# Kernel tuning notes

Measured on AMD Instinct MI355X. Metric: run time of the kernel, lower is better.

The kernel has to match this reference:

```python
import jax, jax.numpy as jnp
import numpy as np

D, ED, N, R, K, NL = 128, 256, 16, 8, 4, 3   # d_model, d_inner, d_state, dt_rank, d_conv, n_layers
B, L = 4, 1024
HID, OUT = 256, 2
EPS = 1e-5


def setup_inputs() -> dict:
    key = jax.random.key(0)
    ks = jax.random.split(key, 16)
    g = lambda k, shape, s=0.05: jax.random.normal(k, shape, dtype=jnp.float32) * s
    return {
        "x": jax.random.normal(ks[0], (B, L, D), dtype=jnp.float32),
        # Mamba params, stacked over (2 directions, NL layers)
        "rms_w": jnp.ones((2, NL, D), jnp.float32),
        "in_w": g(ks[1], (2, NL, 2 * ED, D)),
        "in_b": g(ks[2], (2, NL, 2 * ED)),
        "conv_w": g(ks[3], (2, NL, ED, K)),
        "conv_b": g(ks[4], (2, NL, ED)),
        "xproj_w": g(ks[5], (2, NL, R + 2 * N, ED)),
        "dt_w": g(ks[6], (2, NL, ED, R)),
        "dt_b": g(ks[7], (2, NL, ED)),
        "A_log": jnp.broadcast_to(jnp.log(jnp.arange(1.0, N + 1.0, dtype=jnp.float32)), (2, NL, ED, N)) + 0.0,
        "Dp": jnp.ones((2, NL, ED), jnp.float32),
        "out_w": g(ks[8], (2, NL, D, ED)),
        "out_b": g(ks[9], (2, NL, D)),
        # MLP head params (BatchNorm in training mode: batch stats)
        "bn1_g": jnp.ones((2 * D,), jnp.float32), "bn1_b": jnp.zeros((2 * D,), jnp.float32),
        "w1": g(ks[10], (HID, 2 * D)), "b1": g(ks[11], (HID,)),
        "bn2_g": jnp.ones((HID,), jnp.float32), "bn2_b": jnp.zeros((HID,), jnp.float32),
        "w2": g(ks[12], (HID, HID)), "b2": g(ks[13], (HID,)),
        "bn3_g": jnp.ones((HID,), jnp.float32), "bn3_b": jnp.zeros((HID,), jnp.float32),
        "w3": g(ks[14], (OUT, HID)), "b3": g(ks[15], (OUT,)),
    }


def _rms(x, w):
    return x * jax.lax.rsqrt(jnp.mean(x * x, axis=-1, keepdims=True) + EPS) * w


def _dwconv(x, w, b):
    # causal depthwise conv; x: (B,L,ED), w: (ED,K)
    y = jax.lax.conv_general_dilated(x.transpose(0, 2, 1), w[:, None, :], (1,), [(K - 1, 0)],
                                     feature_group_count=ED, dimension_numbers=("NCH", "OIH", "NCH"))
    return y.transpose(0, 2, 1) + b


def _ssm(dA, dBx, C):
    # dA,dBx: (B,L,ED,N); C: (B,L,N) -> y: (B,L,ED)
    def step(h, inp):
        a, bx, c = inp
        h = a * h + bx
        return h, jnp.einsum("ben,bn->be", h, c)
    h0 = jnp.zeros((dA.shape[0], ED, N), dA.dtype)
    _, ys = jax.lax.scan(step, h0, (dA.transpose(1, 0, 2, 3), dBx.transpose(1, 0, 2, 3), C.transpose(1, 0, 2)))
    return ys.transpose(1, 0, 2)


def _block(x, in_w, in_b, conv_w, conv_b, xproj_w, dt_w, dt_b, A_log, Dp, out_w, out_b):
    xz = x @ in_w.T + in_b
    xi, z = xz[..., :ED], xz[..., ED:]
    xi = jax.nn.silu(_dwconv(xi, conv_w, conv_b))
    dbc = xi @ xproj_w.T
    dt, Bm, Cm = dbc[..., :R], dbc[..., R:R + N], dbc[..., R + N:]
    delta = jax.nn.softplus(dt @ dt_w.T + dt_b)            # (B,L,ED)
    A = -jnp.exp(A_log)                                    # (ED,N)
    dA = jnp.exp(delta[..., None] * A)                     # (B,L,ED,N)
    dBx = (delta * xi)[..., None] * Bm[:, :, None, :]      # (B,L,ED,N)
    y = _ssm(dA, dBx, Cm) + Dp * xi
    y = y * jax.nn.silu(z)
    return y @ out_w.T + out_b


def _mamba(x, d, rms_w, in_w, in_b, conv_w, conv_b, xproj_w, dt_w, dt_b, A_log, Dp, out_w, out_b):
    for l in range(NL):
        x = x + _block(_rms(x, rms_w[d, l]), in_w[d, l], in_b[d, l], conv_w[d, l], conv_b[d, l],
                       xproj_w[d, l], dt_w[d, l], dt_b[d, l], A_log[d, l], Dp[d, l], out_w[d, l], out_b[d, l])
    return x


def _bn(x, g, b):
    m = jnp.mean(x, axis=0)
    v = jnp.mean((x - m) ** 2, axis=0)  # biased var, torch BN training mode
    return (x - m) * jax.lax.rsqrt(v + EPS) * g + b


def _forward(x, rms_w, in_w, in_b, conv_w, conv_b, xproj_w, dt_w, dt_b, A_log, Dp, out_w, out_b,
             bn1_g, bn1_b, w1, b1, bn2_g, bn2_b, w2, b2, bn3_g, bn3_b, w3, b3):
    mp = (rms_w, in_w, in_b, conv_w, conv_b, xproj_w, dt_w, dt_b, A_log, Dp, out_w, out_b)
    fwd = _mamba(x, 0, *mp)
    bwd = jnp.flip(_mamba(jnp.flip(x, axis=1), 1, *mp), axis=1)
    h = jnp.concatenate([fwd, bwd], axis=2).reshape(B * L, 2 * D)
    h = jax.nn.leaky_relu(_bn(h, bn1_g, bn1_b) @ w1.T + b1)
    h = jax.nn.leaky_relu(_bn(h, bn2_g, bn2_b) @ w2.T + b2)
    h = _bn(h, bn3_g, bn3_b) @ w3.T + b3
    return h.reshape(B, L, OUT)


def reference(x, rms_w, in_w, in_b, conv_w, conv_b, xproj_w, dt_w, dt_b, A_log, Dp, out_w, out_b,
              bn1_g, bn1_b, w1, b1, bn2_g, bn2_b, w2, b2, bn3_g, bn3_b, w3, b3):
    return _forward(x, rms_w, in_w, in_b, conv_w, conv_b, xproj_w, dt_w, dt_b, A_log, Dp, out_w, out_b,
                    bn1_g, bn1_b, w1, b1, bn2_g, bn2_b, w2, b2, bn3_g, bn3_b, w3, b3)
```

## Files before the change

### kernel.cpp

```cpp
#include <hip/hip_runtime.h>
#include <hip/hip_bf16.h>
#include <hip/hip_fp16.h>

#define NL 3
#define EPS 1e-5f

#define C_INB    393984L
#define C_CONVW  397056L
#define C_CONVB  403200L
#define C_XPROJW 404736L
#define C_DTW    466176L
#define C_DTB    478464L
#define C_ALOG   480000L
#define C_DP     504576L
#define C_OUTB   702720L
#define C_BN1G   703488L
#define C_BN1B   703744L
#define C_B1     769536L
#define C_BN2G   769792L
#define C_BN2B   770048L
#define C_B2     835840L
#define C_BN3G   836096L
#define C_BN3B   836352L
#define C_W3     836608L
#define C_B3     837120L
#define FLAG_OFF 837184L
#define X0_OFF   837248L
#define X1_OFF   1361536L
#define XZT_OFF  1885824L
#define XCP_OFF  6080128L
#define DBCT_OFF 8177280L
#define YGP_OFF  8504960L
#define BNA_OFF  10603648L
#define HINW_OFF  10605184L
#define HOUTW_OFF 10801792L
#define HW1_OFF   10900096L
#define HW2_OFF   10932864L
#define H1_OFF   XZT_OFF
#define H2_OFF   (XZT_OFF + 1048576L)

#define ASLD 68

struct Ptrs { const void* p[25]; };

typedef _Float16 half8 __attribute__((ext_vector_type(8)));
typedef float f32x4 __attribute__((ext_vector_type(4)));

static __device__ const int  CV_SRC[21] = {0,0,3,4,5,6,7,8,9,10,12,13,14,16,17,18,20,21,22,23,24};
static __device__ const long CV_DST[21] = {X0_OFF,X1_OFF,C_INB,C_CONVW,C_CONVB,C_XPROJW,C_DTW,C_DTB,C_ALOG,C_DP,
                                           C_OUTB,C_BN1G,C_BN1B,C_B1,C_BN2G,C_BN2B,C_B2,C_BN3G,C_BN3B,C_W3,C_B3};
static __device__ const int  CV_SZ[21]  = {524288,524288,3072,6144,1536,61440,12288,1536,24576,1536,
                                           768,256,256,256,256,256,256,256,256,512,2};

__device__ inline float ldsrc(const void* s, long i, bool isbf) {
  if (isbf) { unsigned int u = ((const unsigned short*)s)[i]; return __uint_as_float(u << 16); }
  return ((const float*)s)[i];
}

__global__ __launch_bounds__(256) void g_convert(Ptrs ps, float* __restrict__ ws) {
  bool isbf = (*(const unsigned int*)ps.p[1]) == 0x3F803F80u;
  int job = blockIdx.y;
  if (job == 0 && blockIdx.x == 0 && threadIdx.x == 0) ws[FLAG_OFF] = isbf ? 1.f : 0.f;
  int tid0 = blockIdx.x * 256 + threadIdx.x;
  int stride = gridDim.x * 256;
  if (job < 21) {
    int n = CV_SZ[job];
    const void* s = ps.p[CV_SRC[job]];
    float* dp = ws + CV_DST[job];
    bool permute = (job < 2);
    for (int i = tid0; i < n; i += stride) {
      long si = i;
      if (permute) {
        int row = i >> 7, col = i & 127;
        int b = row >> 10, p = row & 1023;
        int t = ((p & 63) << 4) + (p >> 6);
        si = ((long)((b << 10) + t) << 7) + col;
      }
      dp[i] = ldsrc(s, si, isbf);
    }
  } else if (job == 21) {
    _Float16* dp = (_Float16*)(ws + HINW_OFF);
    const void* sw = ps.p[2]; const void* sr = ps.p[1];
    for (int i = tid0; i < 393216; i += stride) {
      int dl = i >> 16, k = i & 127;
      float v = ldsrc(sw, i, isbf) * ldsrc(sr, dl*128 + k, isbf);
      dp[i] = (_Float16)v;
    }
  } else if (job == 22) {
    _Float16* dp = (_Float16*)(ws + HOUTW_OFF);
    const void* s = ps.p[11];
    for (int i = tid0; i < 196608; i += stride) dp[i] = (_Float16)ldsrc(s, i, isbf);
  } else if (job == 23) {
    _Float16* dp = (_Float16*)(ws + HW1_OFF);
    const void* s = ps.p[15];
    for (int i = tid0; i < 65536; i += stride) dp[i] = (_Float16)ldsrc(s, i, isbf);
  } else if (job == 24) {
    _Float16* dp = (_Float16*)(ws + HW2_OFF);
    const void* s = ps.p[19];
    for (int i = tid0; i < 65536; i += stride) dp[i] = (_Float16)ldsrc(s, i, isbf);
  } else {
    for (int i = tid0; i < 1536; i += stride) ws[BNA_OFF + i] = 0.f;
  }
}

__device__ inline void mm_inner(const float* As, const float* Bs, float4* acc) {
  int tx = threadIdx.x & 15, ty = threadIdx.x >> 4;
  #pragma unroll
  for (int k = 0; k < 64; ++k) {
    float4 av = *(const float4*)&As[k*ASLD + ty*4];
    float4 bv = *(const float4*)&Bs[k*ASLD + tx*4];
    acc[0].x = fmaf(av.x,bv.x,acc[0].x); acc[0].y = fmaf(av.x,bv.y,acc[0].y); acc[0].z = fmaf(av.x,bv.z,acc[0].z); acc[0].w = fmaf(av.x,bv.w,acc[0].w);
    acc[1].x = fmaf(av.y,bv.x,acc[1].x); acc[1].y = fmaf(av.y,bv.y,acc[1].y); acc[1].z = fmaf(av.y,bv.z,acc[1].z); acc[1].w = fmaf(av.y,bv.w,acc[1].w);
    acc[2].x = fmaf(av.z,bv.x,acc[2].x); acc[2].y = fmaf(av.z,bv.y,acc[2].y); acc[2].z = fmaf(av.z,bv.z,acc[2].z); acc[2].w = fmaf(av.z,bv.w,acc[2].w);
    acc[3].x = fmaf(av.w,bv.x,acc[3].x); acc[3].y = fmaf(av.w,bv.y,acc[3].y); acc[3].z = fmaf(av.w,bv.z,acc[3].z); acc[3].w = fmaf(av.w,bv.w,acc[3].w);
  }
}

__device__ inline void stageT_g(float* S, const float* src, int ld, int row0, int k0, int nvalid) {
  int m = threadIdx.x >> 2, q = threadIdx.x & 3;
  const float* p = src + (long)(row0 + m) * ld + k0 + q*16;
  bool ok = (row0 + m) < nvalid;
  #pragma unroll
  for (int j = 0; j < 4; ++j) {
    float4 v = ok ? *(const float4*)(p + j*4) : make_float4(0.f,0.f,0.f,0.f);
    int kk = q*16 + j*4;
    S[(kk+0)*ASLD+m] = v.x; S[(kk+1)*ASLD+m] = v.y; S[(kk+2)*ASLD+m] = v.z; S[(kk+3)*ASLD+m] = v.w;
  }
}

__device__ inline void stageD(float* S, const float* srcT, long ld, int m0, int k0) {
  int k = threadIdx.x >> 2, q = threadIdx.x & 3;
  const float* p = srcT + (long)(k0 + k) * ld + m0 + q*16;
  float4 v0 = *(const float4*)(p);
  float4 v1 = *(const float4*)(p+4);
  float4 v2 = *(const float4*)(p+8);
  float4 v3 = *(const float4*)(p+12);
  float* s = &S[k*ASLD + q*16];
  *(float4*)(s)    = v0; *(float4*)(s+4)  = v1; *(float4*)(s+8)  = v2; *(float4*)(s+12) = v3;
}

__device__ inline float softplusf(float x) {
  if (x > 20.f) return x;
  return __logf(1.f + __expf(x));
}

__global__ __launch_bounds__(256) void g_k1m(float* __restrict__ ws, int layer) {
  int d = blockIdx.z, nt = blockIdx.y, pt = blockIdx.x;
  const float* X = ws + (d ? X1_OFF : X0_OFF);
  const _Float16* Wf = (const _Float16*)(ws + HINW_OFF) + (long)(d*NL+layer)*65536;
  const float* Bi = ws + C_INB + (d*NL+layer)*512;
  __shared__ float rsq[256];
  __shared__ float rsc[64];
  int p0 = pt*64;
  {
    int row = threadIdx.x >> 2, q = threadIdx.x & 3;
    const float* xp = X + (long)(p0+row)*128 + q*32;
    float s = 0.f;
    #pragma unroll
    for (int j = 0; j < 8; ++j) {
      float4 v = *(const float4*)(xp + j*4);
      s += v.x*v.x + v.y*v.y + v.z*v.z + v.w*v.w;
    }
    rsq[row*4+q] = s;
  }
  __syncthreads();
  if (threadIdx.x < 64) {
    float s = rsq[threadIdx.x*4] + rsq[threadIdx.x*4+1] + rsq[threadIdx.x*4+2] + rsq[threadIdx.x*4+3];
    rsc[threadIdx.x] = rsqrtf(s * (1.f/128.f) + EPS);
  }
  __syncthreads();
  int w = threadIdx.x >> 6, lane = threadIdx.x & 63;
  int quad = lane >> 4, lm = lane & 15;
  int n0 = nt*64 + w*16;
  f32x4 zero = {0.f,0.f,0.f,0.f};
  f32x4 acc[4] = {zero, zero, zero, zero};
  #pragma unroll
  for (int s = 0; s < 4; ++s) {
    int k0 = s*32 + quad*8;
    half8 af = *(const half8*)(Wf + (long)(n0+lm)*128 + k0);
    #pragma unroll
    for (int t = 0; t < 4; ++t) {
      int pr = t*16 + lm;
      const float* xp = X + (long)(p0+pr)*128 + k0;
      float4 v0 = *(const float4*)xp;
      float4 v1 = *(const float4*)(xp+4);
      float r = rsc[pr];
      half8 bf;
      bf[0]=(_Float16)(v0.x*r); bf[1]=(_Float16)(v0.y*r); bf[2]=(_Float16)(v0.z*r); bf[3]=(_Float16)(v0.w*r);
      bf[4]=(_Float16)(v1.x*r); bf[5]=(_Float16)(v1.y*r); bf[6]=(_Float16)(v1.z*r); bf[7]=(_Float16)(v1.w*r);
      acc[t] = __builtin_amdgcn_mfma_f32_16x16x32_f16(af, bf, acc[t], 0, 0, 0);
    }
  }
  float* xzt = ws + XZT_OFF + (long)d*2097152L;
  #pragma unroll
  for (int r = 0; r < 4; ++r) {
    int n = n0 + quad*4 + r;
    float bias = Bi[n];
    #pragma unroll
    for (int t = 0; t < 4; ++t) {
      int p = p0 + t*16 + lm;
      xzt[(long)n*4096 + p] = acc[t][r] + bias;
    }
  }
}

__global__ __launch_bounds__(256) void g_k2(float* __restrict__ ws, int layer) {
  int e = blockIdx.x, d = blockIdx.y;
  const float* xrow = ws + XZT_OFF + (long)d*2097152L + (long)e*4096;
  float* orow = ws + XCP_OFF + (long)d*1048576L + (long)e*4096;
  __shared__ float s1[4*1040];
  __shared__ float s2[4*1040];
  int tid = threadIdx.x;
  #pragma unroll
  for (int r = 0; r < 16; ++r) {
    int g = r*256 + tid;
    int b = g >> 10, p = g & 1023;
    int s = (p >> 6)*65 + (p & 63);
    s1[b*1040 + s] = xrow[g];
  }
  __syncthreads();
  float4 wv = *(const float4*)(ws + C_CONVW + (long)((d*NL+layer)*256 + e) * 4);
  float cb = ws[C_CONVB + (d*NL+layer)*256 + e];
  #pragma unroll
  for (int r = 0; r < 16; ++r) {
    int tg = r*256 + tid;
    int b = tg >> 10, tl = tg & 1023;
    const float* st = s1 + b*1040;
    #define SIDX(t) (((t)&15)*65 + ((t)>>4))
    float a = cb;
    if (d == 0) {
      float x0 = (tl >= 3) ? st[SIDX(tl-3)] : 0.f;
      float x1 = (tl >= 2) ? st[SIDX(tl-2)] : 0.f;
      float x2 = (tl >= 1) ? st[SIDX(tl-1)] : 0.f;
      float x3 = st[SIDX(tl)];
      a += wv.x*x0 + wv.y*x1 + wv.z*x2 + wv.w*x3;
    } else {
      float x0 = (tl <= 1020) ? st[SIDX(tl+3)] : 0.f;
      float x1 = (tl <= 1021) ? st[SIDX(tl+2)] : 0.f;
      float x2 = (tl <= 1022) ? st[SIDX(tl+1)] : 0.f;
      float x3 = st[SIDX(tl)];
      a += wv.x*x0 + wv.y*x1 + wv.z*x2 + wv.w*x3;
    }
    #undef SIDX
    s2[b*1040 + ((tl & 15)*65 + (tl >> 4))] = a / (1.f + __expf(-a));
  }
  __syncthreads();
  #pragma unroll
  for (int r = 0; r < 16; ++r) {
    int g = r*256 + tid;
    int b = g >> 10, p = g & 1023;
    orow[g] = s2[b*1040 + (p >> 6)*65 + (p & 63)];
  }
}

__global__ __launch_bounds__(256) void g_k3(float* __restrict__ ws, int layer) {
  int d = blockIdx.z, mt = blockIdx.x;
  int m0 = mt * 64;
  const float* srcT = ws + XCP_OFF + (long)d*1048576L;
  const float* W = ws + C_XPROJW + (long)((d*NL+layer)*40) * 256;
  __shared__ float As[64*ASLD];
  __shared__ float Bs[64*ASLD];
  float4 acc[4] = {make_float4(0,0,0,0),make_float4(0,0,0,0),make_float4(0,0,0,0),make_float4(0,0,0,0)};
  for (int kt = 0; kt < 4; ++kt) {
    stageD(As, srcT, 4096L, m0, kt*64);
    stageT_g(Bs, W, 256, 0, kt*64, 40);
    __syncthreads();
    mm_inner(As, Bs, acc);
    __syncthreads();
  }
  int tx = threadIdx.x & 15, ty = threadIdx.x >> 4;
  #pragma unroll
  for (int i = 0; i < 4; ++i) {
    const float* av = (const float*)&acc[i];
    #pragma unroll
    for (int cc = 0; cc < 4; ++cc) {
      Bs[(tx*4+cc)*65 + ty*4+i] = av[cc];
    }
  }
  __syncthreads();
  float* dbcT = ws + DBCT_OFF + (long)d*163840L;
  #pragma unroll
  for (int r = 0; r < 10; ++r) {
    int el = r*256 + threadIdx.x;
    int n = el >> 6, m = el & 63;
    dbcT[(long)n*4096 + m0 + m] = Bs[n*65 + m];
  }
}

__global__ __launch_bounds__(256) void g_k5(float* __restrict__ ws, int layer) {
  int d = blockIdx.z, b = blockIdx.y, eg = blockIdx.x;
  int es = threadIdx.x >> 6;
  int c  = threadIdx.x & 63;
  int e = eg*4 + es;
  int g0 = b*1024 + c;
  const float* xcp = ws + XCP_OFF + (long)d*1048576L + (long)e*4096 + g0;
  const float* zp  = ws + XZT_OFF + (long)d*2097152L + (long)(256+e)*4096 + g0;
  const float* dbc = ws + DBCT_OFF + (long)d*163840L + g0;
  float*       yo  = ws + YGP_OFF + (long)d*1048576L + (long)e*4096 + g0;
  const float* dw = ws + C_DTW + (long)((d*NL+layer)*256 + e)*8;
  float dtb = ws[C_DTB + (d*NL+layer)*256 + e];
  const float* al = ws + C_ALOG + (long)((d*NL+layer)*256 + e)*16;
  float Dpe = ws[C_DP + (d*NL+layer)*256 + e];
  float dtw[8];
  #pragma unroll
  for (int n = 0; n < 8; ++n) dtw[n] = dw[n];
  float Anv[16]; bool fast = true;
  #pragma unroll
  for (int n = 0; n < 16; ++n) {
    Anv[n] = -__expf(al[n]);
    fast = fast && (fabsf(Anv[n] + (float)(n+1)) < 1e-3f * (float)(n+1));
  }
  __shared__ float aL[4*64*17];
  __shared__ float hL[4*64*17];
  float h[16], ap[16], del[16], xcv[16];
  float Q = 1.f;
  #pragma unroll
  for (int n = 0; n < 16; ++n) { h[n] = 0.f; ap[n] = 1.f; }
  int i0 = d ? 15 : 0, di = d ? -1 : 1;
  for (int s = 0; s < 16; ++s) {
    int i = i0 + s*di;
    int off = i*64;
    float a0 = dtb;
    #pragma unroll
    for (int n = 0; n < 8; ++n) a0 += dbc[(long)n*4096 + off] * dtw[n];
    float dl = softplusf(a0);
    float xc = xcp[off];
    del[s] = dl; xcv[s] = xc;
    float dx = dl * xc;
    if (fast) {
      float q = __expf(-dl);
      float qp[16];
      qp[0]=q; qp[1]=q*q; qp[2]=qp[1]*q; qp[3]=qp[1]*qp[1];
      float q4=qp[3];
      qp[4]=qp[0]*q4; qp[5]=qp[1]*q4; qp[6]=qp[2]*q4; qp[7]=q4*q4;
      float q8=qp[7];
      #pragma unroll
      for (int j = 0; j < 8; ++j) qp[8+j]=qp[j]*q8;
      Q *= q;
      #pragma unroll
      for (int n = 0; n < 16; ++n)
        h[n] = fmaf(qp[n], h[n], dx * dbc[(long)(8+n)*4096 + off]);
    } else {
      #pragma unroll
      for (int n = 0; n < 16; ++n) {
        float a = __expf(dl * Anv[n]);
        ap[n] *= a;
        h[n] = fmaf(a, h[n], dx * dbc[(long)(8+n)*4096 + off]);
      }
    }
  }
  if (fast) {
    float p = Q;
    #pragma unroll
    for (int n = 0; n < 16; ++n) { ap[n] = p; p *= Q; }
  }
  int base = (es*64 + c)*17;
  #pragma unroll
  for (int n = 0; n < 16; ++n) { aL[base+n] = ap[n]; hL[base+n] = h[n]; }
  __syncthreads();
  if (threadIdx.x < 64) {
    int e2 = threadIdx.x >> 4, n = threadIdx.x & 15;
    float h0 = 0.f;
    for (int s2 = 0; s2 < 64; ++s2) {
      int cc = d ? (63 - s2) : s2;
      int ix = (e2*64 + cc)*17 + n;
      float ta = aL[ix], th = hL[ix];
      aL[ix] = h0;
      h0 = fmaf(ta, h0, th);
    }
  }
  __syncthreads();
  #pragma unroll
  for (int n = 0; n < 16; ++n) h[n] = aL[base+n];
  for (int s = 0; s < 16; ++s) {
    int i = i0 + s*di;
    int off = i*64;
    float dl = del[s], xc = xcv[s];
    float dx = dl * xc;
    float zr = zp[off];
    float zg = zr / (1.f + __expf(-zr));
    float ya[4] = {0.f,0.f,0.f,0.f};
    if (fast) {
      float q = __expf(-dl);
      float qp[16];
      qp[0]=q; qp[1]=q*q; qp[2]=qp[1]*q; qp[3]=qp[1]*qp[1];
      float q4=qp[3];
      qp[4]=qp[0]*q4; qp[5]=qp[1]*q4; qp[6]=qp[2]*q4; qp[7]=q4*q4;
      float q8=qp[7];
      #pragma unroll
      for (int j = 0; j < 8; ++j) qp[8+j]=qp[j]*q8;
      #pragma unroll
      for (int n = 0; n < 16; ++n) {
        h[n] = fmaf(qp[n], h[n], dx * dbc[(long)(8+n)*4096 + off]);
        ya[n & 3] = fmaf(h[n], dbc[(long)(24+n)*4096 + off], ya[n & 3]);
      }
    } else {
      #pragma unroll
      for (int n = 0; n < 16; ++n) {
        float a = __expf(dl * Anv[n]);
        h[n] = fmaf(a, h[n], dx * dbc[(long)(8+n)*4096 + off]);
        ya[n & 3] = fmaf(h[n], dbc[(long)(24+n)*4096 + off], ya[n & 3]);
      }
    }
    float y = (ya[0] + ya[1]) + (ya[2] + ya[3]);
    y = fmaf(Dpe, xc, y);
    yo[off] = y * zg;
  }
}

__global__ __launch_bounds__(256) void g_k6m(float* __restrict__ ws, int layer) {
  int d = blockIdx.z, pt = blockIdx.x;
  int p0 = pt*16;
  const float* Y = ws + YGP_OFF + (long)d*1048576L;
  const _Float16* Wf = (const _Float16*)(ws + HOUTW_OFF) + (long)(d*NL+layer)*32768;
  const float* Ob = ws + C_OUTB + (d*NL+layer)*128;
  float* Xd = ws + (d ? X1_OFF : X0_OFF);
  __shared__ __align__(16) _Float16 Ah[16*264];
  {
    int e = threadIdx.x;
    const float* yp = Y + (long)e*4096 + p0;
    float4 v0 = *(const float4*)yp;
    float4 v1 = *(const float4*)(yp+4);
    float4 v2 = *(const float4*)(yp+8);
    float4 v3 = *(const float4*)(yp+12);
    float vv[16] = {v0.x,v0.y,v0.z,v0.w, v1.x,v1.y,v1.z,v1.w,
                    v2.x,v2.y,v2.z,v2.w, v3.x,v3.y,v3.z,v3.w};
    #pragma unroll
    for (int p = 0; p < 16; ++p) Ah[p*264 + e] = (_Float16)vv[p];
  }
  __syncthreads();
  int w = threadIdx.x >> 6, lane = threadIdx.x & 63;
  int quad = lane >> 4, lm = lane & 15;
  f32x4 zero = {0.f,0.f,0.f,0.f};
  f32x4 acc[2] = {zero, zero};
  #pragma unroll
  for (int s = 0; s < 8; ++s) {
    int k0 = s*32 + quad*8;
    half8 af = *(const half8*)(&Ah[lm*264 + k0]);
    #pragma unroll
    for (int t = 0; t < 2; ++t) {
      int n = w*32 + t*16 + lm;
      half8 bf = *(const half8*)(Wf + (long)n*256 + k0);
      acc[t] = __builtin_amdgcn_mfma_f32_16x16x32_f16(af, bf, acc[t], 0, 0, 0);
    }
  }
  bool dostats = (layer == NL-1);
  float* bna = ws + BNA_OFF;
  #pragma unroll
  for (int t = 0; t < 2; ++t) {
    int n = w*32 + t*16 + lm;
    float ob = Ob[n];
    float s1 = 0.f, s2 = 0.f;
    #pragma unroll
    for (int r = 0; r < 4; ++r) {
      int p = p0 + quad*4 + r;
      float v = acc[t][r] + ob + Xd[(long)p*128 + n];
      Xd[(long)p*128 + n] = v;
      s1 += v; s2 += v*v;
    }
    if (dostats) {
      s1 += __shfl_xor(s1, 16, 64); s2 += __shfl_xor(s2, 16, 64);
      s1 += __shfl_xor(s1, 32, 64); s2 += __shfl_xor(s2, 32, 64);
      if (quad == 0) {
        int ch = d*128 + n;
        atomicAdd(&bna[ch], s1);
        atomicAdd(&bna[256 + ch], s2);
      }
    }
  }
}

template<int STAGE>
__global__ __launch_bounds__(256) void g_hgm(float* __restrict__ ws) {
  int p0 = blockIdx.x * 16;
  __shared__ float scL[256], shL[256];
  {
    int k = threadIdx.x;
    float S = ws[BNA_OFF + STAGE*512 + k], S2 = ws[BNA_OFF + STAGE*512 + 256 + k];
    float mean = S * (1.f/4096.f);
    float var = S2 * (1.f/4096.f) - mean*mean;
    const float* g = ws + (STAGE == 0 ? C_BN1G : C_BN2G);
    const float* bb = ws + (STAGE == 0 ? C_BN1B : C_BN2B);
    float sc = g[k] * rsqrtf(var + EPS);
    scL[k] = sc; shL[k] = bb[k] - mean*sc;
  }
  __syncthreads();
  const _Float16* Wf = (const _Float16*)(ws + (STAGE == 0 ? HW1_OFF : HW2_OFF));
  const float* bias = ws + (STAGE == 0 ? C_B1 : C_B2);
  float* H = ws + (STAGE == 0 ? H1_OFF : H2_OFF);
  int w = threadIdx.x >> 6, lane = threadIdx.x & 63;
  int quad = lane >> 4, lm = lane & 15;
  f32x4 zero = {0.f,0.f,0.f,0.f};
  f32x4 acc[4] = {zero, zero, zero, zero};
  #pragma unroll
  for (int s = 0; s < 8; ++s) {
    int k0 = s*32 + quad*8;
    const float* src;
    if (STAGE == 0) src = (k0 < 128) ? (ws + X0_OFF + (long)(p0+lm)*128 + k0)
                                     : (ws + X1_OFF + (long)(p0+lm)*128 + (k0-128));
    else            src = ws + H1_OFF + (long)(p0+lm)*256 + k0;
    float4 v0 = *(const float4*)src, v1 = *(const float4*)(src+4);
    float4 c0 = *(const float4*)&scL[k0], c1 = *(const float4*)&scL[k0+4];
    float4 h0 = *(const float4*)&shL[k0], h1 = *(const float4*)&shL[k0+4];
    half8 af;
    af[0]=(_Float16)(v0.x*c0.x+h0.x); af[1]=(_Float16)(v0.y*c0.y+h0.y);
    af[2]=(_Float16)(v0.z*c0.z+h0.z); af[3]=(_Float16)(v0.w*c0.w+h0.w);
    af[4]=(_Float16)(v1.x*c1.x+h1.x); af[5]=(_Float16)(v1.y*c1.y+h1.y);
    af[6]=(_Float16)(v1.z*c1.z+h1.z); af[7]=(_Float16)(v1.w*c1.w+h1.w);
    #pragma unroll
    for (int t = 0; t < 4; ++t) {
      int n = w*64 + t*16 + lm;
      half8 bf = *(const half8*)(Wf + (long)n*256 + k0);
      acc[t] = __builtin_amdgcn_mfma_f32_16x16x32_f16(af, bf, acc[t], 0, 0, 0);
    }
  }
  float* bna = ws + BNA_OFF + (STAGE+1)*512;
  #pragma unroll
  for (int t = 0; t < 4; ++t) {
    int n = w*64 + t*16 + lm;
    float bs = bias[n];
    float s1 = 0.f, s2 = 0.f;
    #pragma unroll
    for (int r = 0; r < 4; ++r) {
      int p = p0 + quad*4 + r;
      float v = acc[t][r] + bs;
      v = v > 0.f ? v : 0.01f*v;
      H[(long)p*256 + n] = v;
      s1 += v; s2 += v*v;
    }
    s1 += __shfl_xor(s1, 16, 64); s2 += __shfl_xor(s2, 16, 64);
    s1 += __shfl_xor(s1, 32, 64); s2 += __shfl_xor(s2, 32, 64);
    if (quad == 0) {
      atomicAdd(&bna[n], s1);
      atomicAdd(&bna[256 + n], s2);
    }
  }
}

__global__ __launch_bounds__(256) void g_hg2(float* __restrict__ ws, void* dout) {
  int mt = blockIdx.x;
  __shared__ float As[64*ASLD];
  __shared__ float Bs[64*ASLD];
  __shared__ float scL[256], shL[256];
  {
    int k = threadIdx.x;
    float S = ws[BNA_OFF + 2*512 + k], S2 = ws[BNA_OFF + 2*512 + 256 + k];
    float mean = S * (1.f/4096.f);
    float var = S2 * (1.f/4096.f) - mean*mean;
    float sc = ws[C_BN3G + k] * rsqrtf(var + EPS);
    scL[k] = sc; shL[k] = ws[C_BN3B + k] - mean*sc;
  }
  __syncthreads();
  float4 acc[4] = {make_float4(0,0,0,0),make_float4(0,0,0,0),make_float4(0,0,0,0),make_float4(0,0,0,0)};
  for (int kt = 0; kt < 4; ++kt) {
    int k0 = kt * 64;
    {
      int m = threadIdx.x >> 2, q = threadIdx.x & 3;
      const float* p = ws + H2_OFF + (long)(mt*64 + m)*256 + k0 + q*16;
      #pragma unroll
      for (int j = 0; j < 4; ++j) {
        float4 v  = *(const float4*)(p + j*4);
        float4 s4 = *(const float4*)&scL[k0 + q*16 + j*4];
        float4 h4 = *(const float4*)&shL[k0 + q*16 + j*4];
        int kk = q*16 + j*4;
        As[(kk+0)*ASLD+m] = v.x*s4.x + h4.x; As[(kk+1)*ASLD+m] = v.y*s4.y + h4.y;
        As[(kk+2)*ASLD+m] = v.z*s4.z + h4.z; As[(kk+3)*ASLD+m] = v.w*s4.w + h4.w;
      }
    }
    stageT_g(Bs, ws + C_W3, 256, 0, k0, 2);
    __syncthreads();
    mm_inner(As, Bs, acc);
    __syncthreads();
  }
  int tx = threadIdx.x & 15, ty = threadIdx.x >> 4;
  if (tx == 0) {
    bool isbf = ws[FLAG_OFF] != 0.f;
    float b0 = ws[C_B3], b1 = ws[C_B3 + 1];
    #pragma unroll
    for (int i = 0; i < 4; ++i) {
      int r = mt*64 + ty*4 + i;
      int b = r >> 10, p = r & 1023;
      int t = ((p & 63) << 4) + (p >> 6);
      long tok = (long)(b << 10) + t;
      float v0 = acc[i].x + b0, v1 = acc[i].y + b1;
      if (isbf) {
        __hip_bfloat16* o = (__hip_bfloat16*)dout;
        o[tok*2]   = __float2bfloat16(v0);
        o[tok*2+1] = __float2bfloat16(v1);
      } else {
        float* o = (float*)dout;
        o[tok*2] = v0; o[tok*2+1] = v1;
      }
    }
  }
}

extern "C" void kernel_launch(void* const* d_in, const int* in_sizes, int n_in,
                              void* d_out, int out_size, void* d_ws, size_t ws_size,
                              hipStream_t stream) {
  (void)in_sizes; (void)n_in; (void)out_size; (void)ws_size;
  float* ws = (float*)d_ws;
  Ptrs ps;
  for (int i = 0; i < 25; ++i) ps.p[i] = d_in[i];
  g_convert<<<dim3(32, 26), dim3(256), 0, stream>>>(ps, ws);
  for (int l = 0; l < NL; ++l) {
    g_k1m<<<dim3(64, 8, 2), dim3(256), 0, stream>>>(ws, l);
    g_k2 <<<dim3(256, 2),   dim3(256), 0, stream>>>(ws, l);
    g_k3 <<<dim3(64, 1, 2), dim3(256), 0, stream>>>(ws, l);
    g_k5 <<<dim3(64, 4, 2), dim3(256), 0, stream>>>(ws, l);
    g_k6m<<<dim3(256, 1, 2), dim3(256), 0, stream>>>(ws, l);
  }
  g_hgm<0><<<dim3(256), dim3(256), 0, stream>>>(ws);
  g_hgm<1><<<dim3(256), dim3(256), 0, stream>>>(ws);
  g_hg2<<<dim3(64), dim3(256), 0, stream>>>(ws, d_out);
}
```

Measured before the change: 433.6 us.

## Fuse depthwise conv into x-proj and scan kernels, fuse next-layer in_proj into out_proj

```diff
diff --git a/kernel.cpp b/kernel.cpp
--- a/kernel.cpp
+++ b/kernel.cpp
@@ -28,7 +28,6 @@
 #define X0_OFF   837248L
 #define X1_OFF   1361536L
 #define XZT_OFF  1885824L
-#define XCP_OFF  6080128L
 #define DBCT_OFF 8177280L
 #define YGP_OFF  8504960L
 #define BNA_OFF  10603648L
@@ -128,21 +127,11 @@
   }
 }
 
-__device__ inline void stageD(float* S, const float* srcT, long ld, int m0, int k0) {
-  int k = threadIdx.x >> 2, q = threadIdx.x & 3;
-  const float* p = srcT + (long)(k0 + k) * ld + m0 + q*16;
-  float4 v0 = *(const float4*)(p);
-  float4 v1 = *(const float4*)(p+4);
-  float4 v2 = *(const float4*)(p+8);
-  float4 v3 = *(const float4*)(p+12);
-  float* s = &S[k*ASLD + q*16];
-  *(float4*)(s)    = v0; *(float4*)(s+4)  = v1; *(float4*)(s+8)  = v2; *(float4*)(s+12) = v3;
-}
-
 __device__ inline float softplusf(float x) {
   if (x > 20.f) return x;
   return __logf(1.f + __expf(x));
 }
+__device__ inline float siluf(float a) { return a / (1.f + __expf(-a)); }
 
 __global__ __launch_bounds__(256) void g_k1m(float* __restrict__ ws, int layer) {
   int d = blockIdx.z, nt = blockIdx.y, pt = blockIdx.x;
@@ -204,65 +193,47 @@
   }
 }
 
-__global__ __launch_bounds__(256) void g_k2(float* __restrict__ ws, int layer) {
-  int e = blockIdx.x, d = blockIdx.y;
-  const float* xrow = ws + XZT_OFF + (long)d*2097152L + (long)e*4096;
-  float* orow = ws + XCP_OFF + (long)d*1048576L + (long)e*4096;
-  __shared__ float s1[4*1040];
-  __shared__ float s2[4*1040];
-  int tid = threadIdx.x;
-  #pragma unroll
-  for (int r = 0; r < 16; ++r) {
-    int g = r*256 + tid;
-    int b = g >> 10, p = g & 1023;
-    int s = (p >> 6)*65 + (p & 63);
-    s1[b*1040 + s] = xrow[g];
-  }
-  __syncthreads();
-  float4 wv = *(const float4*)(ws + C_CONVW + (long)((d*NL+layer)*256 + e) * 4);
-  float cb = ws[C_CONVB + (d*NL+layer)*256 + e];
-  #pragma unroll
-  for (int r = 0; r < 16; ++r) {
-    int tg = r*256 + tid;
-    int b = tg >> 10, tl = tg & 1023;
-    const float* st = s1 + b*1040;
-    #define SIDX(t) (((t)&15)*65 + ((t)>>4))
-    float a = cb;
-    if (d == 0) {
-      float x0 = (tl >= 3) ? st[SIDX(tl-3)] : 0.f;
-      float x1 = (tl >= 2) ? st[SIDX(tl-2)] : 0.f;
-      float x2 = (tl >= 1) ? st[SIDX(tl-1)] : 0.f;
-      float x3 = st[SIDX(tl)];
-      a += wv.x*x0 + wv.y*x1 + wv.z*x2 + wv.w*x3;
-    } else {
-      float x0 = (tl <= 1020) ? st[SIDX(tl+3)] : 0.f;
-      float x1 = (tl <= 1021) ? st[SIDX(tl+2)] : 0.f;
-      float x2 = (tl <= 1022) ? st[SIDX(tl+1)] : 0.f;
-      float x3 = st[SIDX(tl)];
-      a += wv.x*x0 + wv.y*x1 + wv.z*x2 + wv.w*x3;
-    }
-    #undef SIDX
-    s2[b*1040 + ((tl & 15)*65 + (tl >> 4))] = a / (1.f + __expf(-a));
-  }
-  __syncthreads();
-  #pragma unroll
-  for (int r = 0; r < 16; ++r) {
-    int g = r*256 + tid;
-    int b = g >> 10, p = g & 1023;
-    orow[g] = s2[b*1040 + (p >> 6)*65 + (p & 63)];
-  }
-}
-
-__global__ __launch_bounds__(256) void g_k3(float* __restrict__ ws, int layer) {
+__global__ __launch_bounds__(256) void g_k3c(float* __restrict__ ws, int layer) {
   int d = blockIdx.z, mt = blockIdx.x;
   int m0 = mt * 64;
-  const float* srcT = ws + XCP_OFF + (long)d*1048576L;
+  int bb = mt >> 4, ii = mt & 15;
+  const float* xzbase = ws + XZT_OFF + (long)d*2097152L;
   const float* W = ws + C_XPROJW + (long)((d*NL+layer)*40) * 256;
+  const float* cw = ws + C_CONVW + (long)(d*NL+layer)*1024;
+  const float* cbp = ws + C_CONVB + (d*NL+layer)*256;
   __shared__ float As[64*ASLD];
   __shared__ float Bs[64*ASLD];
+  int colb[4]; int edge[4];
+  #pragma unroll
+  for (int j = 0; j < 4; ++j) {
+    if (d == 0) {
+      int iq = ii - j;
+      if (iq >= 0) { colb[j] = iq*64; edge[j] = 0; }
+      else         { colb[j] = (iq+16)*64 - 1; edge[j] = 1; }
+    } else {
+      int iq = ii + j;
+      if (iq <= 15) { colb[j] = iq*64; edge[j] = 0; }
+      else          { colb[j] = (iq-16)*64 + 1; edge[j] = 2; }
+    }
+  }
+  int m = threadIdx.x & 63, er = threadIdx.x >> 6;
   float4 acc[4] = {make_float4(0,0,0,0),make_float4(0,0,0,0),make_float4(0,0,0,0),make_float4(0,0,0,0)};
   for (int kt = 0; kt < 4; ++kt) {
-    stageD(As, srcT, 4096L, m0, kt*64);
+    for (int pass = 0; pass < 16; ++pass) {
+      int el = pass*4 + er;
+      int e = kt*64 + el;
+      const float* xr = xzbase + (long)e*4096 + bb*1024;
+      float4 cwv = *(const float4*)(cw + e*4);
+      float cb = cbp[e];
+      float xv[4];
+      #pragma unroll
+      for (int j = 0; j < 4; ++j) {
+        bool msk = (edge[j] == 1 && m == 0) || (edge[j] == 2 && m == 63);
+        xv[j] = msk ? 0.f : xr[colb[j] + m];
+      }
+      float a = cb + cwv.w*xv[0] + cwv.z*xv[1] + cwv.y*xv[2] + cwv.x*xv[3];
+      As[el*ASLD + m] = siluf(a);
+    }
     stageT_g(Bs, W, 256, 0, kt*64, 40);
     __syncthreads();
     mm_inner(As, Bs, acc);
@@ -282,25 +253,27 @@
   #pragma unroll
   for (int r = 0; r < 10; ++r) {
     int el = r*256 + threadIdx.x;
-    int n = el >> 6, m = el & 63;
-    dbcT[(long)n*4096 + m0 + m] = Bs[n*65 + m];
-  }
-}
-
-__global__ __launch_bounds__(256) void g_k5(float* __restrict__ ws, int layer) {
+    int n = el >> 6, mm = el & 63;
+    dbcT[(long)n*4096 + m0 + mm] = Bs[n*65 + mm];
+  }
+}
+
+__global__ __launch_bounds__(256) void g_k5c(float* __restrict__ ws, int layer) {
   int d = blockIdx.z, b = blockIdx.y, eg = blockIdx.x;
   int es = threadIdx.x >> 6;
   int c  = threadIdx.x & 63;
   int e = eg*4 + es;
   int g0 = b*1024 + c;
-  const float* xcp = ws + XCP_OFF + (long)d*1048576L + (long)e*4096 + g0;
-  const float* zp  = ws + XZT_OFF + (long)d*2097152L + (long)(256+e)*4096 + g0;
+  const float* xzrow = ws + XZT_OFF + (long)d*2097152L + (long)e*4096 + g0;
+  const float* zp    = ws + XZT_OFF + (long)d*2097152L + (long)(256+e)*4096 + g0;
   const float* dbc = ws + DBCT_OFF + (long)d*163840L + g0;
   float*       yo  = ws + YGP_OFF + (long)d*1048576L + (long)e*4096 + g0;
   const float* dw = ws + C_DTW + (long)((d*NL+layer)*256 + e)*8;
   float dtb = ws[C_DTB + (d*NL+layer)*256 + e];
   const float* al = ws + C_ALOG + (long)((d*NL+layer)*256 + e)*16;
   float Dpe = ws[C_DP + (d*NL+layer)*256 + e];
+  float4 cwv = *(const float4*)(ws + C_CONVW + (long)((d*NL+layer)*256 + e)*4);
+  float cb = ws[C_CONVB + (d*NL+layer)*256 + e];
   float dtw[8];
   #pragma unroll
   for (int n = 0; n < 8; ++n) dtw[n] = dw[n];
@@ -309,6 +282,14 @@
   for (int n = 0; n < 16; ++n) {
     Anv[n] = -__expf(al[n]);
     fast = fast && (fabsf(Anv[n] + (float)(n+1)) < 1e-3f * (float)(n+1));
+  }
+  float w1, w2, w3;
+  if (d == 0) {
+    if (c > 0) { w1 = xzrow[959]; w2 = xzrow[895]; w3 = xzrow[831]; }
+    else { w1 = w2 = w3 = 0.f; }
+  } else {
+    if (c < 63) { w1 = xzrow[1]; w2 = xzrow[65]; w3 = xzrow[129]; }
+    else { w1 = w2 = w3 = 0.f; }
   }
   __shared__ float aL[4*64*17];
   __shared__ float hL[4*64*17];
@@ -324,7 +305,9 @@
     #pragma unroll
     for (int n = 0; n < 8; ++n) a0 += dbc[(long)n*4096 + off] * dtw[n];
     float dl = softplusf(a0);
-    float xc = xcp[off];
+    float xt = xzrow[off];
+    float xc = siluf(cb + cwv.w*xt + cwv.z*w1 + cwv.y*w2 + cwv.x*w3);
+    w3 = w2; w2 = w1; w1 = xt;
     del[s] = dl; xcv[s] = xc;
     float dx = dl * xc;
     if (fast) {
@@ -408,7 +391,7 @@
   }
 }
 
-__global__ __launch_bounds__(256) void g_k6m(float* __restrict__ ws, int layer) {
+__global__ __launch_bounds__(256) void g_k61(float* __restrict__ ws, int layer) {
   int d = blockIdx.z, pt = blockIdx.x;
   int p0 = pt*16;
   const float* Y = ws + YGP_OFF + (long)d*1048576L;
@@ -416,6 +399,9 @@
   const float* Ob = ws + C_OUTB + (d*NL+layer)*128;
   float* Xd = ws + (d ? X1_OFF : X0_OFF);
   __shared__ __align__(16) _Float16 Ah[16*264];
+  __shared__ float Xn[16*137];
+  __shared__ float rsq[64];
+  __shared__ float rsc[16];
   {
     int e = threadIdx.x;
     const float* yp = Y + (long)e*4096 + p0;
@@ -456,6 +442,7 @@
       int p = p0 + quad*4 + r;
       float v = acc[t][r] + ob + Xd[(long)p*128 + n];
       Xd[(long)p*128 + n] = v;
+      Xn[(quad*4 + r)*137 + n] = v;
       s1 += v; s2 += v*v;
     }
     if (dostats) {
@@ -466,6 +453,49 @@
         atomicAdd(&bna[ch], s1);
         atomicAdd(&bna[256 + ch], s2);
       }
+    }
+  }
+  if (layer == NL-1) return;
+  __syncthreads();
+  if (threadIdx.x < 64) {
+    int pl = threadIdx.x >> 2, qq = threadIdx.x & 3;
+    float s = 0.f;
+    const float* xr = &Xn[pl*137 + qq*32];
+    #pragma unroll
+    for (int k = 0; k < 32; ++k) s += xr[k]*xr[k];
+    rsq[threadIdx.x] = s;
+  }
+  __syncthreads();
+  if (threadIdx.x < 16) {
+    float s = rsq[threadIdx.x*4] + rsq[threadIdx.x*4+1] + rsq[threadIdx.x*4+2] + rsq[threadIdx.x*4+3];
+    rsc[threadIdx.x] = rsqrtf(s * (1.f/128.f) + EPS);
+  }
+  __syncthreads();
+  const _Float16* Wn = (const _Float16*)(ws + HINW_OFF) + (long)(d*NL+layer+1)*65536;
+  const float* Bi = ws + C_INB + (d*NL+layer+1)*512;
+  f32x4 acc2[8] = {zero,zero,zero,zero,zero,zero,zero,zero};
+  float r = rsc[lm];
+  #pragma unroll
+  for (int s = 0; s < 4; ++s) {
+    int k0 = s*32 + quad*8;
+    half8 bf;
+    const float* xr = &Xn[lm*137 + k0];
+    #pragma unroll
+    for (int j = 0; j < 8; ++j) bf[j] = (_Float16)(xr[j] * r);
+    #pragma unroll
+    for (int tt = 0; tt < 8; ++tt) {
+      int n2 = w*128 + tt*16 + lm;
+      half8 af = *(const half8*)(Wn + (long)n2*128 + k0);
+      acc2[tt] = __builtin_amdgcn_mfma_f32_16x16x32_f16(af, bf, acc2[tt], 0, 0, 0);
+    }
+  }
+  float* xzt = ws + XZT_OFF + (long)d*2097152L;
+  #pragma unroll
+  for (int tt = 0; tt < 8; ++tt) {
+    #pragma unroll
+    for (int rr = 0; rr < 4; ++rr) {
+      int n2 = w*128 + tt*16 + quad*4 + rr;
+      xzt[(long)n2*4096 + p0 + lm] = acc2[tt][rr] + Bi[n2];
     }
   }
 }
@@ -603,12 +633,11 @@
   Ptrs ps;
   for (int i = 0; i < 25; ++i) ps.p[i] = d_in[i];
   g_convert<<<dim3(32, 26), dim3(256), 0, stream>>>(ps, ws);
+  g_k1m<<<dim3(64, 8, 2), dim3(256), 0, stream>>>(ws, 0);
   for (int l = 0; l < NL; ++l) {
-    g_k1m<<<dim3(64, 8, 2), dim3(256), 0, stream>>>(ws, l);
-    g_k2 <<<dim3(256, 2),   dim3(256), 0, stream>>>(ws, l);
-    g_k3 <<<dim3(64, 1, 2), dim3(256), 0, stream>>>(ws, l);
-    g_k5 <<<dim3(64, 4, 2), dim3(256), 0, stream>>>(ws, l);
-    g_k6m<<<dim3(256, 1, 2), dim3(256), 0, stream>>>(ws, l);
+    g_k3c<<<dim3(64, 1, 2), dim3(256), 0, stream>>>(ws, l);
+    g_k5c<<<dim3(64, 4, 2), dim3(256), 0, stream>>>(ws, l);
+    g_k61<<<dim3(256, 1, 2), dim3(256), 0, stream>>>(ws, l);
   }
   g_hgm<0><<<dim3(256), dim3(256), 0, stream>>>(ws);
   g_hgm<1><<<dim3(256), dim3(256), 0, stream>>>(ws);
```

Result: slower. 468.7 us (+8.1%).
